# Optimization experiments

Measured on AMD Instinct MI355X. Metric: run time of the kernel, lower is better.

## Reference

```python
import jax, jax.numpy as jnp
import numpy as np

N_NODES = 100000
N_EDGES = 1600000
IN_C, HID_C, OUT_C = 128, 128, 40


def setup_inputs() -> dict:
    key = jax.random.key(0)
    ks = jax.random.split(key, 10)
    def lin(k, fin, fout):
        return jax.random.normal(k, (fin, fout), jnp.float32) / np.sqrt(fin).astype(np.float32)
    return {
        "x": jax.random.normal(ks[0], (N_NODES, IN_C), jnp.float32),
        "edge_index": jax.random.randint(ks[1], (2, N_EDGES), 0, N_NODES, jnp.int64),
        "W1a": lin(ks[2], IN_C, HID_C), "b1a": jnp.zeros((HID_C,), jnp.float32),
        "W1b": lin(ks[3], HID_C, HID_C), "b1b": jnp.zeros((HID_C,), jnp.float32),
        "W2a": lin(ks[4], HID_C, HID_C), "b2a": jnp.zeros((HID_C,), jnp.float32),
        "W2b": lin(ks[5], HID_C, OUT_C), "b2b": jnp.zeros((OUT_C,), jnp.float32),
    }


def gin_conv(x, edge_index, Wa, ba, Wb, bb):
    # GINConv with eps=0: h_i = MLP(x_i + sum_{j in N(i)} x_j)
    src, dst = edge_index[0], edge_index[1]
    agg = jax.ops.segment_sum(x[src], dst, num_segments=N_NODES)  # [N, C]
    h = x + agg
    h = jnp.maximum(h @ Wa + ba, 0.0)  # Linear + ReLU
    return h @ Wb + bb                 # Linear


def reference(x, edge_index, W1a, b1a, W1b, b1b, W2a, b2a, W2b, b2b):
    h = gin_conv(x, edge_index, W1a, b1a, W1b, b1b)
    h = jnp.maximum(h, 0.0)
    # dropout(p=0.5) treated as identity (eval mode / deterministic reference)
    h = gin_conv(h, edge_index, W2a, b2a, W2b, b2b)
    return jax.nn.log_softmax(h, axis=1)
```

## Files before the change

### kernel.cpp

```cpp
#include <hip/hip_runtime.h>

#define N_NODES 100000
#define N_EDGES 1600000
#define CH 128
#define OUTC 40
#define CAP 64
#define NBKT 98
#define BKT_CAP 18432
#define P1_EDGES 4096
#define ROW4 16
#define QROW2 16
#define QSCALE (6.5f / 127.0f)
#define QINV   (127.0f / 6.5f)
#define ZROW N_NODES

typedef __attribute__((ext_vector_type(8))) short bf16x8s;
typedef __attribute__((ext_vector_type(4))) float f32x4;

__device__ __forceinline__ unsigned short f2b_rne(float f) {
    union { float f; unsigned int u; } c; c.f = f;
    unsigned int r = (c.u + 0x7FFF + ((c.u >> 16) & 1)) >> 16;
    return (unsigned short)r;
}
__device__ __forceinline__ float b2f(unsigned short b) {
    union { float f; unsigned int u; } c; c.u = ((unsigned int)b) << 16;
    return c.f;
}
__device__ __forceinline__ int q8(float f) {
    return __float2int_rn(fminf(fmaxf(f * QINV, -127.f), 127.f));
}

__global__ __launch_bounds__(256) void conv_f32_bf16_i8(const float4* __restrict__ in,
                                                        ushort4* __restrict__ outb,
                                                        uint2* __restrict__ outq, int n8) {
    int i = blockIdx.x * 256 + threadIdx.x;
    if (i >= n8) return;
    float4 a = in[i * 2], b = in[i * 2 + 1];
    ushort4 o0, o1;
    o0.x = f2b_rne(a.x); o0.y = f2b_rne(a.y); o0.z = f2b_rne(a.z); o0.w = f2b_rne(a.w);
    o1.x = f2b_rne(b.x); o1.y = f2b_rne(b.y); o1.z = f2b_rne(b.z); o1.w = f2b_rne(b.w);
    outb[i * 2] = o0; outb[i * 2 + 1] = o1;
    uint2 q;
    q.x = (unsigned)((q8(a.x) + 128) & 0xFF) | (((unsigned)((q8(a.y) + 128) & 0xFF)) << 8) |
          (((unsigned)((q8(a.z) + 128) & 0xFF)) << 16) | (((unsigned)((q8(a.w) + 128) & 0xFF)) << 24);
    q.y = (unsigned)((q8(b.x) + 128) & 0xFF) | (((unsigned)((q8(b.y) + 128) & 0xFF)) << 8) |
          (((unsigned)((q8(b.z) + 128) & 0xFF)) << 16) | (((unsigned)((q8(b.w) + 128) & 0xFF)) << 24);
    outq[i] = q;
}

__global__ __launch_bounds__(256) void setup_misc(int* __restrict__ gcursor,
                                                  unsigned int* __restrict__ xq,
                                                  unsigned int* __restrict__ h1q) {
    int t = threadIdx.x;
    if (t < NBKT) gcursor[t] = 0;
    if (t >= 128 && t < 160) {
        int i = t - 128;
        xq[(size_t)ZROW * 32 + i] = 0x80808080u;
        h1q[(size_t)ZROW * 32 + i] = 0x80808080u;
    }
}

__global__ __launch_bounds__(256) void bin_edges(const int* __restrict__ esrc,
                                                 const int* __restrict__ edst,
                                                 int* __restrict__ gcursor,
                                                 unsigned int* __restrict__ bins) {
    __shared__ uint2 stage[P1_EDGES];
    __shared__ int lcnt[NBKT];
    __shared__ int lofs[NBKT];
    __shared__ int lpos[NBKT];
    __shared__ int gbase[NBKT];
    const int tid = threadIdx.x;
    const int e0 = blockIdx.x * P1_EDGES;

    for (int i = tid; i < NBKT; i += 256) lcnt[i] = 0;
    __syncthreads();

    int s[16], d[16];
#pragma unroll
    for (int i = 0; i < 16; ++i) {
        int e = e0 + i * 256 + tid;
        if (e < N_EDGES) { s[i] = esrc[e]; d[i] = edst[e]; }
        else d[i] = -1;
    }
#pragma unroll
    for (int i = 0; i < 16; ++i)
        if (d[i] >= 0) atomicAdd(&lcnt[d[i] >> 10], 1);
    __syncthreads();

    if (tid < NBKT) lofs[tid] = lcnt[tid];
    __syncthreads();
    for (int dd = 1; dd < NBKT; dd <<= 1) {
        int v = 0;
        if (tid < NBKT && tid >= dd) v = lofs[tid - dd];
        __syncthreads();
        if (tid < NBKT) lofs[tid] += v;
        __syncthreads();
    }
    if (tid < NBKT) {
        lpos[tid] = lofs[tid] - lcnt[tid];
        gbase[tid] = atomicAdd(&gcursor[tid], lcnt[tid]);
    }
    __syncthreads();

#pragma unroll
    for (int i = 0; i < 16; ++i) {
        if (d[i] >= 0) {
            int b = d[i] >> 10;
            int slot = atomicAdd(&lpos[b], 1);
            stage[slot] = make_uint2((unsigned)s[i], (unsigned)d[i]);
        }
    }
    __syncthreads();

    int total = lofs[NBKT - 1];
    for (int r = tid; r < total; r += 256) {
        uint2 rec = stage[r];
        int b = (int)(rec.y >> 10);
        int excl = lofs[b] - lcnt[b];
        int pos = gbase[b] + (r - excl);
        unsigned p = ((rec.y & 1023u) << 17) | rec.x;
        if (pos < BKT_CAP) bins[(size_t)b * BKT_CAP + pos] = p;
    }
}

__global__ __launch_bounds__(256) void build_from_bins(const unsigned int* __restrict__ bins,
                                                       const int* __restrict__ gcursor,
                                                       int* __restrict__ adj,
                                                       int* __restrict__ cnt) {
    __shared__ int lc[1024];
    const int b = blockIdx.x;
    const int tid = threadIdx.x;
    const int base = b << 10;
    for (int i = tid; i < 1024; i += 256) lc[i] = 0;
    __syncthreads();
    int n = gcursor[b]; if (n > BKT_CAP) n = BKT_CAP;
    const unsigned int* myb = bins + (size_t)b * BKT_CAP;
    for (int i = tid; i < n; i += 256) {
        unsigned p = myb[i];
        int local = (int)(p >> 17);
        int src = (int)(p & 0x1FFFFu);
        int slot = atomicAdd(&lc[local], 1);
        if (slot < CAP) adj[((base + local) << 6) + slot] = src;
    }
    __syncthreads();
    for (int i = tid; i < 1024; i += 256) {
        int node = base + i;
        if (node < N_NODES) {
            int dg = lc[i];
            cnt[node] = dg;
            int s0 = dg > CAP ? CAP : dg;
            int nr = (s0 + 15) & ~15;
            for (int s = s0; s < nr; ++s)
                adj[(node << 6) + s] = ZROW;
        }
    }
}

__global__ __launch_bounds__(256) void pack_w3(const float* __restrict__ W0,
                                               const float* __restrict__ W1,
                                               const float* __restrict__ W2,
                                               unsigned short* __restrict__ P0,
                                               unsigned short* __restrict__ P1,
                                               unsigned short* __restrict__ P2) {
    int t = blockIdx.x * 256 + threadIdx.x;
    if (t >= 3 * 2048) return;
    int which = t >> 11;
    int rem = t & 2047;
    int lane = rem & 63;
    int ks = (rem >> 6) & 3;
    int nt = rem >> 8;
    const float* W = which == 0 ? W0 : (which == 1 ? W1 : W2);
    unsigned short* P = which == 0 ? P0 : (which == 1 ? P1 : P2);
    int n = nt * 16 + (lane & 15);
    int kbase = ks * 32 + (lane >> 4) * 8;
    unsigned short* dst = P + ((nt * 4 + ks) * 64 + lane) * 8;
#pragma unroll
    for (int j = 0; j < 8; ++j)
        dst[j] = f2b_rne(W[(kbase + j) * CH + n]);
}

__global__ __launch_bounds__(256) void pack_wout(const float* __restrict__ W,
                                                 unsigned short* __restrict__ P) {
    int t = blockIdx.x * 256 + threadIdx.x;
    if (t >= 768) return;
    int nt = t >> 8, rem = t & 255;
    int ks = rem >> 6, lane = rem & 63;
    int n = nt * 16 + (lane & 15);
    int kbase = ks * 32 + (lane >> 4) * 8;
    unsigned short* dst = P + ((nt * 4 + ks) * 64 + lane) * 8;
#pragma unroll
    for (int j = 0; j < 8; ++j)
        dst[j] = (n < OUTC) ? f2b_rne(W[(kbase + j) * OUTC + n]) : (unsigned short)0;
}

template <bool FIXED>
__device__ __forceinline__ void gather_u8_body(const unsigned int* __restrict__ xq,
                                               const unsigned short* __restrict__ xb,
                                               const int* __restrict__ adj,
                                               const int* __restrict__ cnt,
                                               const unsigned int* __restrict__ hmax,
                                               unsigned short* __restrict__ agg) {
    int node = blockIdx.x * 4 + (threadIdx.x >> 6);
    int lane = threadIdx.x & 63;
    if (node >= N_NODES) return;
    int grp = lane >> 4, l16 = lane & 15;
    const uint2* q2 = reinterpret_cast<const uint2*>(xq);
    const uint4* f4 = reinterpret_cast<const uint4*>(xb);

    int deg = cnt[node];
    if (deg > CAP) deg = CAP;
    int nr = (deg + 15) & ~15;
    int nb = (lane < nr) ? adj[(node << 6) + lane] : 0;
    uint4 sv = f4[node * ROW4 + l16];

    float dq;
    if (FIXED) dq = QSCALE;
    else {
        union { unsigned u; float f; } c; c.u = hmax[0];
        dq = c.f * (1.0f / 127.0f);
    }

    unsigned a0 = 0, a1 = 0, a2 = 0, a3 = 0;

    for (int j = 0; j < nr; j += 16) {
        int j0 = j + grp;
        int s0 = __shfl(nb, j0, 64);
        int s1 = __shfl(nb, j0 + 4, 64);
        int s2 = __shfl(nb, j0 + 8, 64);
        int s3 = __shfl(nb, j0 + 12, 64);
        uint2 v0 = q2[s0 * QROW2 + l16];
        uint2 v1 = q2[s1 * QROW2 + l16];
        uint2 v2 = q2[s2 * QROW2 + l16];
        uint2 v3 = q2[s3 * QROW2 + l16];
        a0 += __builtin_amdgcn_perm(v0.x, v0.x, 0x0C020C00u);
        a1 += __builtin_amdgcn_perm(v0.x, v0.x, 0x0C030C01u);
        a2 += __builtin_amdgcn_perm(v0.y, v0.y, 0x0C020C00u);
        a3 += __builtin_amdgcn_perm(v0.y, v0.y, 0x0C030C01u);
        a0 += __builtin_amdgcn_perm(v1.x, v1.x, 0x0C020C00u);
        a1 += __builtin_amdgcn_perm(v1.x, v1.x, 0x0C030C01u);
        a2 += __builtin_amdgcn_perm(v1.y, v1.y, 0x0C020C00u);
        a3 += __builtin_amdgcn_perm(v1.y, v1.y, 0x0C030C01u);
        a0 += __builtin_amdgcn_perm(v2.x, v2.x, 0x0C020C00u);
        a1 += __builtin_amdgcn_perm(v2.x, v2.x, 0x0C030C01u);
        a2 += __builtin_amdgcn_perm(v2.y, v2.y, 0x0C020C00u);
        a3 += __builtin_amdgcn_perm(v2.y, v2.y, 0x0C030C01u);
        a0 += __builtin_amdgcn_perm(v3.x, v3.x, 0x0C020C00u);
        a1 += __builtin_amdgcn_perm(v3.x, v3.x, 0x0C030C01u);
        a2 += __builtin_amdgcn_perm(v3.y, v3.y, 0x0C020C00u);
        a3 += __builtin_amdgcn_perm(v3.y, v3.y, 0x0C030C01u);
    }
    a0 += (unsigned)__shfl_xor((int)a0, 16, 64); a0 += (unsigned)__shfl_xor((int)a0, 32, 64);
    a1 += (unsigned)__shfl_xor((int)a1, 16, 64); a1 += (unsigned)__shfl_xor((int)a1, 32, 64);
    a2 += (unsigned)__shfl_xor((int)a2, 16, 64); a2 += (unsigned)__shfl_xor((int)a2, 32, 64);
    a3 += (unsigned)__shfl_xor((int)a3, 16, 64); a3 += (unsigned)__shfl_xor((int)a3, 32, 64);

    if (grp == 0) {
        int bias = nr << 7;
        float q0 = (float)((int)(a0 & 0xFFFFu) - bias);
        float q1 = (float)((int)(a1 & 0xFFFFu) - bias);
        float q2c = (float)((int)(a0 >> 16) - bias);
        float q3 = (float)((int)(a1 >> 16) - bias);
        float q4 = (float)((int)(a2 & 0xFFFFu) - bias);
        float q5 = (float)((int)(a3 & 0xFFFFu) - bias);
        float q6 = (float)((int)(a2 >> 16) - bias);
        float q7 = (float)((int)(a3 >> 16) - bias);
        float r0 = b2f((unsigned short)(sv.x & 0xFFFF)) + dq * q0;
        float r1 = b2f((unsigned short)(sv.x >> 16)) + dq * q1;
        float r2 = b2f((unsigned short)(sv.y & 0xFFFF)) + dq * q2c;
        float r3 = b2f((unsigned short)(sv.y >> 16)) + dq * q3;
        float r4 = b2f((unsigned short)(sv.z & 0xFFFF)) + dq * q4;
        float r5 = b2f((unsigned short)(sv.z >> 16)) + dq * q5;
        float r6 = b2f((unsigned short)(sv.w & 0xFFFF)) + dq * q6;
        float r7 = b2f((unsigned short)(sv.w >> 16)) + dq * q7;
        uint4 o;
        o.x = (unsigned)f2b_rne(r0) | ((unsigned)f2b_rne(r1) << 16);
        o.y = (unsigned)f2b_rne(r2) | ((unsigned)f2b_rne(r3) << 16);
        o.z = (unsigned)f2b_rne(r4) | ((unsigned)f2b_rne(r5) << 16);
        o.w = (unsigned)f2b_rne(r6) | ((unsigned)f2b_rne(r7) << 16);
        reinterpret_cast<uint4*>(agg)[node * ROW4 + l16] = o;
    }
}

__global__ __launch_bounds__(256) void gather_agg_u8(const unsigned int* __restrict__ xq,
                                                     const unsigned short* __restrict__ xb,
                                                     const int* __restrict__ adj,
                                                     const int* __restrict__ cnt,
                                                     unsigned short* __restrict__ agg) {
    gather_u8_body<true>(xq, xb, adj, cnt, nullptr, agg);
}

__global__ __launch_bounds__(256) void gather_agg_u8_dyn(const unsigned int* __restrict__ xq,
                                                         const unsigned short* __restrict__ xb,
                                                         const int* __restrict__ adj,
                                                         const int* __restrict__ cnt,
                                                         const unsigned int* __restrict__ hmax,
                                                         unsigned short* __restrict__ agg) {
    gather_u8_body<false>(xq, xb, adj, cnt, hmax, agg);
}

__global__ __launch_bounds__(256) void reduce_max(const float* __restrict__ bmax, int n,
                                                  unsigned int* __restrict__ hmax) {
    float m = 0.f;
    for (int i = threadIdx.x; i < n; i += 256) m = fmaxf(m, bmax[i]);
#pragma unroll
    for (int off = 1; off < 64; off <<= 1) m = fmaxf(m, __shfl_xor(m, off, 64));
    __shared__ float wm[4];
    if ((threadIdx.x & 63) == 0) wm[threadIdx.x >> 6] = m;
    __syncthreads();
    if (threadIdx.x == 0)
        hmax[0] = __float_as_uint(fmaxf(fmaxf(wm[0], wm[1]), fmaxf(wm[2], wm[3])));
}

__global__ __launch_bounds__(256) void quant_h1(const uint4* __restrict__ h1,
                                                const unsigned int* __restrict__ hmax,
                                                uint2* __restrict__ outq, int n8) {
    int i = blockIdx.x * 256 + threadIdx.x;
    if (i >= n8) return;
    union { unsigned u; float f; } c; c.u = hmax[0];
    float inv = 127.0f / fmaxf(c.f, 1e-30f);
    uint4 v = h1[i];
    int q[8];
    q[0] = __float2int_rn(fminf(b2f((unsigned short)(v.x & 0xFFFF)) * inv, 127.f));
    q[1] = __float2int_rn(fminf(b2f((unsigned short)(v.x >> 16)) * inv, 127.f));
    q[2] = __float2int_rn(fminf(b2f((unsigned short)(v.y & 0xFFFF)) * inv, 127.f));
    q[3] = __float2int_rn(fminf(b2f((unsigned short)(v.y >> 16)) * inv, 127.f));
    q[4] = __float2int_rn(fminf(b2f((unsigned short)(v.z & 0xFFFF)) * inv, 127.f));
    q[5] = __float2int_rn(fminf(b2f((unsigned short)(v.z >> 16)) * inv, 127.f));
    q[6] = __float2int_rn(fminf(b2f((unsigned short)(v.w & 0xFFFF)) * inv, 127.f));
    q[7] = __float2int_rn(fminf(b2f((unsigned short)(v.w >> 16)) * inv, 127.f));
    uint2 o;
    o.x = (unsigned)((q[0] + 128) & 0xFF) | (((unsigned)((q[1] + 128) & 0xFF)) << 8) |
          (((unsigned)((q[2] + 128) & 0xFF)) << 16) | (((unsigned)((q[3] + 128) & 0xFF)) << 24);
    o.y = (unsigned)((q[4] + 128) & 0xFF) | (((unsigned)((q[5] + 128) & 0xFF)) << 8) |
          (((unsigned)((q[6] + 128) & 0xFF)) << 16) | (((unsigned)((q[7] + 128) & 0xFF)) << 24);
    outq[i] = o;
}

__global__ __launch_bounds__(256) void gin_mlp_fused(const unsigned short* __restrict__ A,
                                                     const unsigned short* __restrict__ Pa,
                                                     const float* __restrict__ ba,
                                                     const unsigned short* __restrict__ Pb2,
                                                     const float* __restrict__ bb,
                                                     unsigned short* __restrict__ Cout,
                                                     float* __restrict__ bmax,
                                                     int M) {
    __shared__ unsigned short As[64 * 136];
    __shared__ float sm_max[4];
    const int row0 = blockIdx.x * 64;
    const int tid = threadIdx.x;
    const int wave = tid >> 6;
    const int lane = tid & 63;
    const int quad = lane >> 4;
    const int l15 = lane & 15;
    const int nt0 = wave * 2;

    bf16x8s b1f[2][4];
#pragma unroll
    for (int c = 0; c < 2; ++c)
#pragma unroll
        for (int ks = 0; ks < 4; ++ks)
            b1f[c][ks] = *reinterpret_cast<const bf16x8s*>(
                Pa + (((nt0 + c) * 4 + ks) * 64 + lane) * 8);

    {
        int r = tid & 63, seg = tid >> 6;
        int row = row0 + r;
        uint4 z = make_uint4(0, 0, 0, 0);
        const uint4* src = reinterpret_cast<const uint4*>(A + (long long)row * CH + seg * 32);
        uint4* dst = reinterpret_cast<uint4*>(&As[r * 136 + seg * 32]);
#pragma unroll
        for (int i = 0; i < 4; ++i)
            dst[i] = (row < M) ? src[i] : z;
    }
    __syncthreads();

    f32x4 acc[2][4];
#pragma unroll
    for (int c = 0; c < 2; ++c)
#pragma unroll
        for (int t = 0; t < 4; ++t) acc[c][t] = (f32x4){0.f, 0.f, 0.f, 0.f};
#pragma unroll
    for (int t = 0; t < 4; ++t)
#pragma unroll
        for (int ks = 0; ks < 4; ++ks) {
            bf16x8s af = *reinterpret_cast<const bf16x8s*>(
                &As[(t * 16 + l15) * 136 + ks * 32 + quad * 8]);
            acc[0][t] = __builtin_amdgcn_mfma_f32_16x16x32_bf16(af, b1f[0][ks], acc[0][t], 0, 0, 0);
            acc[1][t] = __builtin_amdgcn_mfma_f32_16x16x32_bf16(af, b1f[1][ks], acc[1][t], 0, 0, 0);
        }

    bf16x8s b2f_[2][4];
#pragma unroll
    for (int c = 0; c < 2; ++c)
#pragma unroll
        for (int ks = 0; ks < 4; ++ks)
            b2f_[c][ks] = *reinterpret_cast<const bf16x8s*>(
                Pb2 + (((nt0 + c) * 4 + ks) * 64 + lane) * 8);

    __syncthreads();
#pragma unroll
    for (int c = 0; c < 2; ++c) {
        int col = (nt0 + c) * 16 + l15;
        float bv = ba[col];
#pragma unroll
        for (int t = 0; t < 4; ++t)
#pragma unroll
            for (int r = 0; r < 4; ++r) {
                int rl = t * 16 + quad * 4 + r;
                As[rl * 136 + col] = f2b_rne(fmaxf(acc[c][t][r] + bv, 0.f));
            }
    }
    __syncthreads();

    f32x4 a2[2][4];
#pragma unroll
    for (int c = 0; c < 2; ++c)
#pragma unroll
        for (int t = 0; t < 4; ++t) a2[c][t] = (f32x4){0.f, 0.f, 0.f, 0.f};
#pragma unroll
    for (int t = 0; t < 4; ++t)
#pragma unroll
        for (int ks = 0; ks < 4; ++ks) {
            bf16x8s af = *reinterpret_cast<const bf16x8s*>(
                &As[(t * 16 + l15) * 136 + ks * 32 + quad * 8]);
            a2[0][t] = __builtin_amdgcn_mfma_f32_16x16x32_bf16(af, b2f_[0][ks], a2[0][t], 0, 0, 0);
            a2[1][t] = __builtin_amdgcn_mfma_f32_16x16x32_bf16(af, b2f_[1][ks], a2[1][t], 0, 0, 0);
        }
    __syncthreads();

    float wmax = 0.f;
#pragma unroll
    for (int c = 0; c < 2; ++c) {
        int col = (nt0 + c) * 16 + l15;
        float bv = bb[col];
#pragma unroll
        for (int t = 0; t < 4; ++t)
#pragma unroll
            for (int r = 0; r < 4; ++r) {
                int rl = t * 16 + quad * 4 + r;
                float v = fmaxf(a2[c][t][r] + bv, 0.f);
                if (row0 + rl < M) wmax = fmaxf(wmax, v);
                As[rl * 136 + col] = f2b_rne(v);
            }
    }
#pragma unroll
    for (int off = 1; off < 64; off <<= 1) wmax = fmaxf(wmax, __shfl_xor(wmax, off, 64));
    if (lane == 0) sm_max[wave] = wmax;
    __syncthreads();

    {
        int r = tid >> 2;
        int q = tid & 3;
        int row = row0 + r;
        if (row < M) {
            uint4* dst = reinterpret_cast<uint4*>(Cout + (long long)row * CH + q * 32);
            const unsigned short* sp = &As[r * 136 + q * 32];
#pragma unroll
            for (int i = 0; i < 4; ++i)
                dst[i] = *reinterpret_cast<const uint4*>(sp + i * 8);
        }
        if (tid == 0)
            bmax[blockIdx.x] = fmaxf(fmaxf(sm_max[0], sm_max[1]),
                                     fmaxf(sm_max[2], sm_max[3]));
    }
}

__global__ __launch_bounds__(256) void gin_out_fused(const unsigned short* __restrict__ A,
                                                     const unsigned short* __restrict__ Pa,
                                                     const float* __restrict__ ba,
                                                     const unsigned short* __restrict__ Pb,
                                                     const float* __restrict__ bias,
                                                     float* __restrict__ out, int M) {
    __shared__ unsigned short As[64 * 136];
    const int row0 = blockIdx.x * 64;
    const int tid = threadIdx.x;
    const int wave = tid >> 6;
    const int lane = tid & 63;
    const int quad = lane >> 4;
    const int l15 = lane & 15;
    const int nt0 = wave * 2;

    bf16x8s b1f[2][4];
#pragma unroll
    for (int c = 0; c < 2; ++c)
#pragma unroll
        for (int ks = 0; ks < 4; ++ks)
            b1f[c][ks] = *reinterpret_cast<const bf16x8s*>(
                Pa + (((nt0 + c) * 4 + ks) * 64 + lane) * 8);

    {
        int r = tid & 63, seg = tid >> 6;
        int row = row0 + r;
        uint4 z = make_uint4(0, 0, 0, 0);
        const uint4* src = reinterpret_cast<const uint4*>(A + (long long)row * CH + seg * 32);
        uint4* dst = reinterpret_cast<uint4*>(&As[r * 136 + seg * 32]);
#pragma unroll
        for (int i = 0; i < 4; ++i)
            dst[i] = (row < M) ? src[i] : z;
    }
    __syncthreads();

    f32x4 acc[2][4];
#pragma unroll
    for (int c = 0; c < 2; ++c)
#pragma unroll
        for (int t = 0; t < 4; ++t) acc[c][t] = (f32x4){0.f, 0.f, 0.f, 0.f};
#pragma unroll
    for (int t = 0; t < 4; ++t)
#pragma unroll
        for (int ks = 0; ks < 4; ++ks) {
            bf16x8s af = *reinterpret_cast<const bf16x8s*>(
                &As[(t * 16 + l15) * 136 + ks * 32 + quad * 8]);
            acc[0][t] = __builtin_amdgcn_mfma_f32_16x16x32_bf16(af, b1f[0][ks], acc[0][t], 0, 0, 0);
            acc[1][t] = __builtin_amdgcn_mfma_f32_16x16x32_bf16(af, b1f[1][ks], acc[1][t], 0, 0, 0);
        }

    bf16x8s bof[3][4];
#pragma unroll
    for (int nt = 0; nt < 3; ++nt)
#pragma unroll
        for (int ks = 0; ks < 4; ++ks)
            bof[nt][ks] = *reinterpret_cast<const bf16x8s*>(
                Pb + ((nt * 4 + ks) * 64 + lane) * 8);

    __syncthreads();
#pragma unroll
    for (int c = 0; c < 2; ++c) {
        int col = (nt0 + c) * 16 + l15;
        float bv = ba[col];
#pragma unroll
        for (int t = 0; t < 4; ++t)
#pragma unroll
            for (int r = 0; r < 4; ++r) {
                int rl = t * 16 + quad * 4 + r;
                As[rl * 136 + col] = f2b_rne(fmaxf(acc[c][t][r] + bv, 0.f));
            }
    }
    __syncthreads();

    f32x4 oacc[3];
#pragma unroll
    for (int nt = 0; nt < 3; ++nt) oacc[nt] = (f32x4){0.f, 0.f, 0.f, 0.f};
#pragma unroll
    for (int ks = 0; ks < 4; ++ks) {
        bf16x8s af = *reinterpret_cast<const bf16x8s*>(
            &As[(wave * 16 + l15) * 136 + ks * 32 + quad * 8]);
#pragma unroll
        for (int nt = 0; nt < 3; ++nt)
            oacc[nt] = __builtin_amdgcn_mfma_f32_16x16x32_bf16(af, bof[nt][ks], oacc[nt], 0, 0, 0);
    }

    const float b0v = bias[l15];
    const float b1v = bias[16 + l15];
    const float b2v = (l15 < 8) ? bias[32 + l15] : 0.f;
#pragma unroll
    for (int r = 0; r < 4; ++r) {
        int row = row0 + wave * 16 + quad * 4 + r;
        float v0 = oacc[0][r] + b0v;
        float v1 = oacc[1][r] + b1v;
        float v2 = (l15 < 8) ? (oacc[2][r] + b2v) : -1e30f;
        float m = fmaxf(fmaxf(v0, v1), v2);
#pragma unroll
        for (int off = 1; off < 16; off <<= 1) m = fmaxf(m, __shfl_xor(m, off, 64));
        float s = __expf(v0 - m) + __expf(v1 - m) + ((l15 < 8) ? __expf(v2 - m) : 0.f);
#pragma unroll
        for (int off = 1; off < 16; off <<= 1) s += __shfl_xor(s, off, 64);
        float lg = m + __logf(s);
        if (row < M) {
            float* orow = out + (long long)row * OUTC;
            orow[l15] = v0 - lg;
            orow[16 + l15] = v1 - lg;
            if (l15 < 8) orow[32 + l15] = v2 - lg;
        }
    }
}

extern "C" void kernel_launch(void* const* d_in, const int* in_sizes, int n_in,
                              void* d_out, int out_size, void* d_ws, size_t ws_size,
                              hipStream_t stream) {
    const float* x   = (const float*)d_in[0];
    const int* eidx  = (const int*)d_in[1];
    const int* esrc  = eidx;
    const int* edst  = eidx + N_EDGES;
    const float* W1a = (const float*)d_in[2];
    const float* b1a = (const float*)d_in[3];
    const float* W1b = (const float*)d_in[4];
    const float* b1b = (const float*)d_in[5];
    const float* W2a = (const float*)d_in[6];
    const float* b2a = (const float*)d_in[7];
    const float* W2b = (const float*)d_in[8];
    const float* b2b = (const float*)d_in[9];
    float* out = (float*)d_out;

    const size_t fe = (size_t)N_NODES * CH;
    const size_t qrow_pad = 32;
    unsigned short* xb  = (unsigned short*)d_ws;
    unsigned short* b0  = xb + fe;
    unsigned short* b1  = b0 + fe;
    unsigned int* xq    = (unsigned int*)(b1 + fe);
    unsigned int* h1q   = xq + fe / 4 + qrow_pad;
    int* adj     = (int*)(h1q + fe / 4 + qrow_pad);
    int* cnt     = adj + (size_t)N_NODES * CAP;
    int* gcursor = cnt + N_NODES;
    unsigned int* hmax = (unsigned int*)(gcursor + NBKT);
    float* bmax = (float*)(hmax + 2);
    unsigned int* bins = (unsigned int*)(bmax + 1568);
    unsigned short* P1 = (unsigned short*)(bins + (size_t)NBKT * BKT_CAP);
    unsigned short* P2 = P1 + 16384;
    unsigned short* P3 = P2 + 16384;
    unsigned short* Pb = P3 + 16384;

    const int conv_grid  = (int)((fe / 8 + 255) / 256);
    const int bin_grid   = (N_EDGES + P1_EDGES - 1) / P1_EDGES;
    const int gath_grid  = (N_NODES + 3) / 4;
    const int gemm_grid  = (N_NODES + 63) / 64;
    const int q8_grid    = (int)((fe / 8 + 255) / 256);

    conv_f32_bf16_i8<<<conv_grid, 256, 0, stream>>>((const float4*)x, (ushort4*)xb,
                                                    (uint2*)xq, (int)(fe / 8));
    setup_misc<<<1, 256, 0, stream>>>(gcursor, xq, h1q);
    bin_edges<<<bin_grid, 256, 0, stream>>>(esrc, edst, gcursor, bins);
    build_from_bins<<<NBKT, 256, 0, stream>>>(bins, gcursor, adj, cnt);
    pack_w3<<<24, 256, 0, stream>>>(W1a, W1b, W2a, P1, P2, P3);
    pack_wout<<<3, 256, 0, stream>>>(W2b, Pb);

    gather_agg_u8<<<gath_grid, 256, 0, stream>>>(xq, xb, adj, cnt, b0);
    gin_mlp_fused<<<gemm_grid, 256, 0, stream>>>(b0, P1, b1a, P2, b1b, b1, bmax, N_NODES);

    reduce_max<<<1, 256, 0, stream>>>(bmax, gemm_grid, hmax);
    quant_h1<<<q8_grid, 256, 0, stream>>>((const uint4*)b1, hmax, (uint2*)h1q, (int)(fe / 8));
    gather_agg_u8_dyn<<<gath_grid, 256, 0, stream>>>(h1q, b1, adj, cnt, hmax, b0);
    gin_out_fused<<<gemm_grid, 256, 0, stream>>>(b0, P3, b2a, Pb, b2b, out, N_NODES);
}
```

Measured before the change: 299.9 us.

## Merge small setup kernels and gather two nodes per wave

Folds the setup_misc zeroing into block 0 of the conversion kernel. Merges the two weight-packing kernels into one and folds the global max reduction into every quant_h1 block, which removes three launches. build_from_bins now runs 1024 threads per bucket and no longer writes ZROW padding, because the gather masks lanes at or beyond the degree to ZROW itself. The gather processes two nodes per wave to raise memory-level parallelism. The cost is that each quant_h1 block re-reads all block maxima, and the pair loop runs to the larger of the two degrees.

```diff
diff --git a/kernel.cpp b/kernel.cpp
--- a/kernel.cpp
+++ b/kernel.cpp
@@ -32,7 +32,19 @@
 
 __global__ __launch_bounds__(256) void conv_f32_bf16_i8(const float4* __restrict__ in,
                                                         ushort4* __restrict__ outb,
-                                                        uint2* __restrict__ outq, int n8) {
+                                                        uint2* __restrict__ outq, int n8,
+                                                        int* __restrict__ gcursor,
+                                                        unsigned int* __restrict__ xqd,
+                                                        unsigned int* __restrict__ h1qd) {
+    if (blockIdx.x == 0) {
+        int t = threadIdx.x;
+        if (t < NBKT) gcursor[t] = 0;
+        if (t >= 128 && t < 160) {
+            int i = t - 128;
+            xqd[(size_t)ZROW * 32 + i] = 0x80808080u;
+            h1qd[(size_t)ZROW * 32 + i] = 0x80808080u;
+        }
+    }
     int i = blockIdx.x * 256 + threadIdx.x;
     if (i >= n8) return;
     float4 a = in[i * 2], b = in[i * 2 + 1];
@@ -48,18 +60,6 @@
     outq[i] = q;
 }
 
-__global__ __launch_bounds__(256) void setup_misc(int* __restrict__ gcursor,
-                                                  unsigned int* __restrict__ xq,
-                                                  unsigned int* __restrict__ h1q) {
-    int t = threadIdx.x;
-    if (t < NBKT) gcursor[t] = 0;
-    if (t >= 128 && t < 160) {
-        int i = t - 128;
-        xq[(size_t)ZROW * 32 + i] = 0x80808080u;
-        h1q[(size_t)ZROW * 32 + i] = 0x80808080u;
-    }
-}
-
 __global__ __launch_bounds__(256) void bin_edges(const int* __restrict__ esrc,
                                                  const int* __restrict__ edst,
                                                  int* __restrict__ gcursor,
@@ -123,19 +123,19 @@
     }
 }
 
-__global__ __launch_bounds__(256) void build_from_bins(const unsigned int* __restrict__ bins,
-                                                       const int* __restrict__ gcursor,
-                                                       int* __restrict__ adj,
-                                                       int* __restrict__ cnt) {
+__global__ __launch_bounds__(1024) void build_from_bins(const unsigned int* __restrict__ bins,
+                                                        const int* __restrict__ gcursor,
+                                                        int* __restrict__ adj,
+                                                        int* __restrict__ cnt) {
     __shared__ int lc[1024];
     const int b = blockIdx.x;
     const int tid = threadIdx.x;
     const int base = b << 10;
-    for (int i = tid; i < 1024; i += 256) lc[i] = 0;
+    lc[tid] = 0;
     __syncthreads();
     int n = gcursor[b]; if (n > BKT_CAP) n = BKT_CAP;
     const unsigned int* myb = bins + (size_t)b * BKT_CAP;
-    for (int i = tid; i < n; i += 256) {
+    for (int i = tid; i < n; i += 1024) {
         unsigned p = myb[i];
         int local = (int)(p >> 17);
         int src = (int)(p & 0x1FFFFu);
@@ -143,54 +143,72 @@
         if (slot < CAP) adj[((base + local) << 6) + slot] = src;
     }
     __syncthreads();
-    for (int i = tid; i < 1024; i += 256) {
-        int node = base + i;
-        if (node < N_NODES) {
-            int dg = lc[i];
-            cnt[node] = dg;
-            int s0 = dg > CAP ? CAP : dg;
-            int nr = (s0 + 15) & ~15;
-            for (int s = s0; s < nr; ++s)
-                adj[(node << 6) + s] = ZROW;
-        }
-    }
-}
-
-__global__ __launch_bounds__(256) void pack_w3(const float* __restrict__ W0,
-                                               const float* __restrict__ W1,
-                                               const float* __restrict__ W2,
-                                               unsigned short* __restrict__ P0,
-                                               unsigned short* __restrict__ P1,
-                                               unsigned short* __restrict__ P2) {
+    {
+        int node = base + tid;
+        if (node < N_NODES) cnt[node] = lc[tid];
+    }
+}
+
+__global__ __launch_bounds__(256) void pack_weights(const float* __restrict__ W0,
+                                                    const float* __restrict__ W1,
+                                                    const float* __restrict__ W2,
+                                                    const float* __restrict__ Wo,
+                                                    unsigned short* __restrict__ P0,
+                                                    unsigned short* __restrict__ P1,
+                                                    unsigned short* __restrict__ P2,
+                                                    unsigned short* __restrict__ Po) {
     int t = blockIdx.x * 256 + threadIdx.x;
-    if (t >= 3 * 2048) return;
-    int which = t >> 11;
-    int rem = t & 2047;
-    int lane = rem & 63;
-    int ks = (rem >> 6) & 3;
-    int nt = rem >> 8;
-    const float* W = which == 0 ? W0 : (which == 1 ? W1 : W2);
-    unsigned short* P = which == 0 ? P0 : (which == 1 ? P1 : P2);
-    int n = nt * 16 + (lane & 15);
-    int kbase = ks * 32 + (lane >> 4) * 8;
-    unsigned short* dst = P + ((nt * 4 + ks) * 64 + lane) * 8;
-#pragma unroll
-    for (int j = 0; j < 8; ++j)
-        dst[j] = f2b_rne(W[(kbase + j) * CH + n]);
-}
-
-__global__ __launch_bounds__(256) void pack_wout(const float* __restrict__ W,
-                                                 unsigned short* __restrict__ P) {
-    int t = blockIdx.x * 256 + threadIdx.x;
-    if (t >= 768) return;
-    int nt = t >> 8, rem = t & 255;
-    int ks = rem >> 6, lane = rem & 63;
-    int n = nt * 16 + (lane & 15);
-    int kbase = ks * 32 + (lane >> 4) * 8;
-    unsigned short* dst = P + ((nt * 4 + ks) * 64 + lane) * 8;
-#pragma unroll
-    for (int j = 0; j < 8; ++j)
-        dst[j] = (n < OUTC) ? f2b_rne(W[(kbase + j) * OUTC + n]) : (unsigned short)0;
+    if (t < 3 * 2048) {
+        int which = t >> 11;
+        int rem = t & 2047;
+        int lane = rem & 63;
+        int ks = (rem >> 6) & 3;
+        int nt = rem >> 8;
+        const float* W = which == 0 ? W0 : (which == 1 ? W1 : W2);
+        unsigned short* P = which == 0 ? P0 : (which == 1 ? P1 : P2);
+        int n = nt * 16 + (lane & 15);
+        int kbase = ks * 32 + (lane >> 4) * 8;
+        unsigned short* dst = P + ((nt * 4 + ks) * 64 + lane) * 8;
+#pragma unroll
+        for (int j = 0; j < 8; ++j)
+            dst[j] = f2b_rne(W[(kbase + j) * CH + n]);
+    } else if (t < 3 * 2048 + 768) {
+        int u = t - 3 * 2048;
+        int nt = u >> 8, rem = u & 255;
+        int ks = rem >> 6, lane = rem & 63;
+        int n = nt * 16 + (lane & 15);
+        int kbase = ks * 32 + (lane >> 4) * 8;
+        unsigned short* dst = Po + ((nt * 4 + ks) * 64 + lane) * 8;
+#pragma unroll
+        for (int j = 0; j < 8; ++j)
+            dst[j] = (n < OUTC) ? f2b_rne(Wo[(kbase + j) * OUTC + n]) : (unsigned short)0;
+    }
+}
+
+__device__ __forceinline__ void gather_epi(unsigned a0, unsigned a1, unsigned a2, unsigned a3,
+                                           uint4 sv, int bias, float dq, uint4* __restrict__ dst) {
+    float q0 = (float)((int)(a0 & 0xFFFFu) - bias);
+    float q1 = (float)((int)(a1 & 0xFFFFu) - bias);
+    float q2 = (float)((int)(a0 >> 16) - bias);
+    float q3 = (float)((int)(a1 >> 16) - bias);
+    float q4 = (float)((int)(a2 & 0xFFFFu) - bias);
+    float q5 = (float)((int)(a3 & 0xFFFFu) - bias);
+    float q6 = (float)((int)(a2 >> 16) - bias);
+    float q7 = (float)((int)(a3 >> 16) - bias);
+    float r0 = b2f((unsigned short)(sv.x & 0xFFFF)) + dq * q0;
+    float r1 = b2f((unsigned short)(sv.x >> 16)) + dq * q1;
+    float r2 = b2f((unsigned short)(sv.y & 0xFFFF)) + dq * q2;
+    float r3 = b2f((unsigned short)(sv.y >> 16)) + dq * q3;
+    float r4 = b2f((unsigned short)(sv.z & 0xFFFF)) + dq * q4;
+    float r5 = b2f((unsigned short)(sv.z >> 16)) + dq * q5;
+    float r6 = b2f((unsigned short)(sv.w & 0xFFFF)) + dq * q6;
+    float r7 = b2f((unsigned short)(sv.w >> 16)) + dq * q7;
+    uint4 o;
+    o.x = (unsigned)f2b_rne(r0) | ((unsigned)f2b_rne(r1) << 16);
+    o.y = (unsigned)f2b_rne(r2) | ((unsigned)f2b_rne(r3) << 16);
+    o.z = (unsigned)f2b_rne(r4) | ((unsigned)f2b_rne(r5) << 16);
+    o.w = (unsigned)f2b_rne(r6) | ((unsigned)f2b_rne(r7) << 16);
+    *dst = o;
 }
 
 template <bool FIXED>
@@ -200,18 +218,24 @@
                                                const int* __restrict__ cnt,
                                                const unsigned int* __restrict__ hmax,
                                                unsigned short* __restrict__ agg) {
-    int node = blockIdx.x * 4 + (threadIdx.x >> 6);
-    int lane = threadIdx.x & 63;
-    if (node >= N_NODES) return;
-    int grp = lane >> 4, l16 = lane & 15;
+    const int wave = threadIdx.x >> 6;
+    const int lane = threadIdx.x & 63;
+    const int node0 = blockIdx.x * 8 + wave * 2;
+    if (node0 >= N_NODES) return;
+    const int grp = lane >> 4, l16 = lane & 15;
     const uint2* q2 = reinterpret_cast<const uint2*>(xq);
     const uint4* f4 = reinterpret_cast<const uint4*>(xb);
 
-    int deg = cnt[node];
-    if (deg > CAP) deg = CAP;
-    int nr = (deg + 15) & ~15;
-    int nb = (lane < nr) ? adj[(node << 6) + lane] : 0;
-    uint4 sv = f4[node * ROW4 + l16];
+    int2 dgp = *reinterpret_cast<const int2*>(cnt + node0);
+    int deg0 = dgp.x > CAP ? CAP : dgp.x;
+    int deg1 = dgp.y > CAP ? CAP : dgp.y;
+    int nr0 = (deg0 + 15) & ~15;
+    int nr1 = (deg1 + 15) & ~15;
+    int nrm = nr0 > nr1 ? nr0 : nr1;
+    int nb0 = (lane < deg0) ? adj[(node0 << 6) + lane] : ZROW;
+    int nb1 = (lane < deg1) ? adj[(node0 << 6) + 64 + lane] : ZROW;
+    uint4 sv0 = f4[node0 * ROW4 + l16];
+    uint4 sv1 = f4[node0 * ROW4 + ROW4 + l16];
 
     float dq;
     if (FIXED) dq = QSCALE;
@@ -220,64 +244,74 @@
         dq = c.f * (1.0f / 127.0f);
     }
 
-    unsigned a0 = 0, a1 = 0, a2 = 0, a3 = 0;
-
-    for (int j = 0; j < nr; j += 16) {
+    unsigned a00 = 0, a01 = 0, a02 = 0, a03 = 0;
+    unsigned a10 = 0, a11 = 0, a12 = 0, a13 = 0;
+
+    for (int j = 0; j < nrm; j += 16) {
         int j0 = j + grp;
-        int s0 = __shfl(nb, j0, 64);
-        int s1 = __shfl(nb, j0 + 4, 64);
-        int s2 = __shfl(nb, j0 + 8, 64);
-        int s3 = __shfl(nb, j0 + 12, 64);
-        uint2 v0 = q2[s0 * QROW2 + l16];
-        uint2 v1 = q2[s1 * QROW2 + l16];
-        uint2 v2 = q2[s2 * QROW2 + l16];
-        uint2 v3 = q2[s3 * QROW2 + l16];
-        a0 += __builtin_amdgcn_perm(v0.x, v0.x, 0x0C020C00u);
-        a1 += __builtin_amdgcn_perm(v0.x, v0.x, 0x0C030C01u);
-        a2 += __builtin_amdgcn_perm(v0.y, v0.y, 0x0C020C00u);
-        a3 += __builtin_amdgcn_perm(v0.y, v0.y, 0x0C030C01u);
-        a0 += __builtin_amdgcn_perm(v1.x, v1.x, 0x0C020C00u);
-        a1 += __builtin_amdgcn_perm(v1.x, v1.x, 0x0C030C01u);
-        a2 += __builtin_amdgcn_perm(v1.y, v1.y, 0x0C020C00u);
-        a3 += __builtin_amdgcn_perm(v1.y, v1.y, 0x0C030C01u);
-        a0 += __builtin_amdgcn_perm(v2.x, v2.x, 0x0C020C00u);
-        a1 += __builtin_amdgcn_perm(v2.x, v2.x, 0x0C030C01u);
-        a2 += __builtin_amdgcn_perm(v2.y, v2.y, 0x0C020C00u);
-        a3 += __builtin_amdgcn_perm(v2.y, v2.y, 0x0C030C01u);
-        a0 += __builtin_amdgcn_perm(v3.x, v3.x, 0x0C020C00u);
-        a1 += __builtin_amdgcn_perm(v3.x, v3.x, 0x0C030C01u);
-        a2 += __builtin_amdgcn_perm(v3.y, v3.y, 0x0C020C00u);
-        a3 += __builtin_amdgcn_perm(v3.y, v3.y, 0x0C030C01u);
-    }
-    a0 += (unsigned)__shfl_xor((int)a0, 16, 64); a0 += (unsigned)__shfl_xor((int)a0, 32, 64);
-    a1 += (unsigned)__shfl_xor((int)a1, 16, 64); a1 += (unsigned)__shfl_xor((int)a1, 32, 64);
-    a2 += (unsigned)__shfl_xor((int)a2, 16, 64); a2 += (unsigned)__shfl_xor((int)a2, 32, 64);
-    a3 += (unsigned)__shfl_xor((int)a3, 16, 64); a3 += (unsigned)__shfl_xor((int)a3, 32, 64);
+        int s00 = __shfl(nb0, j0, 64);
+        int s01 = __shfl(nb0, j0 + 4, 64);
+        int s02 = __shfl(nb0, j0 + 8, 64);
+        int s03 = __shfl(nb0, j0 + 12, 64);
+        int s10 = __shfl(nb1, j0, 64);
+        int s11 = __shfl(nb1, j0 + 4, 64);
+        int s12 = __shfl(nb1, j0 + 8, 64);
+        int s13 = __shfl(nb1, j0 + 12, 64);
+        uint2 v00 = q2[s00 * QROW2 + l16];
+        uint2 v01 = q2[s01 * QROW2 + l16];
+        uint2 v02 = q2[s02 * QROW2 + l16];
+        uint2 v03 = q2[s03 * QROW2 + l16];
+        uint2 v10 = q2[s10 * QROW2 + l16];
+        uint2 v11 = q2[s11 * QROW2 + l16];
+        uint2 v12 = q2[s12 * QROW2 + l16];
+        uint2 v13 = q2[s13 * QROW2 + l16];
+        a00 += __builtin_amdgcn_perm(v00.x, v00.x, 0x0C020C00u);
+        a01 += __builtin_amdgcn_perm(v00.x, v00.x, 0x0C030C01u);
+        a02 += __builtin_amdgcn_perm(v00.y, v00.y, 0x0C020C00u);
+        a03 += __builtin_amdgcn_perm(v00.y, v00.y, 0x0C030C01u);
+        a00 += __builtin_amdgcn_perm(v01.x, v01.x, 0x0C020C00u);
+        a01 += __builtin_amdgcn_perm(v01.x, v01.x, 0x0C030C01u);
+        a02 += __builtin_amdgcn_perm(v01.y, v01.y, 0x0C020C00u);
+        a03 += __builtin_amdgcn_perm(v01.y, v01.y, 0x0C030C01u);
+        a00 += __builtin_amdgcn_perm(v02.x, v02.x, 0x0C020C00u);
+        a01 += __builtin_amdgcn_perm(v02.x, v02.x, 0x0C030C01u);
+        a02 += __builtin_amdgcn_perm(v02.y, v02.y, 0x0C020C00u);
+        a03 += __builtin_amdgcn_perm(v02.y, v02.y, 0x0C030C01u);
+        a00 += __builtin_amdgcn_perm(v03.x, v03.x, 0x0C020C00u);
+        a01 += __builtin_amdgcn_perm(v03.x, v03.x, 0x0C030C01u);
+        a02 += __builtin_amdgcn_perm(v03.y, v03.y, 0x0C020C00u);
+        a03 += __builtin_amdgcn_perm(v03.y, v03.y, 0x0C030C01u);
+        a10 += __builtin_amdgcn_perm(v10.x, v10.x, 0x0C020C00u);
+        a11 += __builtin_amdgcn_perm(v10.x, v10.x, 0x0C030C01u);
+        a12 += __builtin_amdgcn_perm(v10.y, v10.y, 0x0C020C00u);
+        a13 += __builtin_amdgcn_perm(v10.y, v10.y, 0x0C030C01u);
+        a10 += __builtin_amdgcn_perm(v11.x, v11.x, 0x0C020C00u);
+        a11 += __builtin_amdgcn_perm(v11.x, v11.x, 0x0C030C01u);
+        a12 += __builtin_amdgcn_perm(v11.y, v11.y, 0x0C020C00u);
+        a13 += __builtin_amdgcn_perm(v11.y, v11.y, 0x0C030C01u);
+        a10 += __builtin_amdgcn_perm(v12.x, v12.x, 0x0C020C00u);
+        a11 += __builtin_amdgcn_perm(v12.x, v12.x, 0x0C030C01u);
+        a12 += __builtin_amdgcn_perm(v12.y, v12.y, 0x0C020C00u);
+        a13 += __builtin_amdgcn_perm(v12.y, v12.y, 0x0C030C01u);
+        a10 += __builtin_amdgcn_perm(v13.x, v13.x, 0x0C020C00u);
+        a11 += __builtin_amdgcn_perm(v13.x, v13.x, 0x0C030C01u);
+        a12 += __builtin_amdgcn_perm(v13.y, v13.y, 0x0C020C00u);
+        a13 += __builtin_amdgcn_perm(v13.y, v13.y, 0x0C030C01u);
+    }
+    a00 += (unsigned)__shfl_xor((int)a00, 16, 64); a00 += (unsigned)__shfl_xor((int)a00, 32, 64);
+    a01 += (unsigned)__shfl_xor((int)a01, 16, 64); a01 += (unsigned)__shfl_xor((int)a01, 32, 64);
+    a02 += (unsigned)__shfl_xor((int)a02, 16, 64); a02 += (unsigned)__shfl_xor((int)a02, 32, 64);
+    a03 += (unsigned)__shfl_xor((int)a03, 16, 64); a03 += (unsigned)__shfl_xor((int)a03, 32, 64);
+    a10 += (unsigned)__shfl_xor((int)a10, 16, 64); a10 += (unsigned)__shfl_xor((int)a10, 32, 64);
+    a11 += (unsigned)__shfl_xor((int)a11, 16, 64); a11 += (unsigned)__shfl_xor((int)a11, 32, 64);
+    a12 += (unsigned)__shfl_xor((int)a12, 16, 64); a12 += (unsigned)__shfl_xor((int)a12, 32, 64);
+    a13 += (unsigned)__shfl_xor((int)a13, 16, 64); a13 += (unsigned)__shfl_xor((int)a13, 32, 64);
 
     if (grp == 0) {
-        int bias = nr << 7;
-        float q0 = (float)((int)(a0 & 0xFFFFu) - bias);
-        float q1 = (float)((int)(a1 & 0xFFFFu) - bias);
-        float q2c = (float)((int)(a0 >> 16) - bias);
-        float q3 = (float)((int)(a1 >> 16) - bias);
-        float q4 = (float)((int)(a2 & 0xFFFFu) - bias);
-        float q5 = (float)((int)(a3 & 0xFFFFu) - bias);
-        float q6 = (float)((int)(a2 >> 16) - bias);
-        float q7 = (float)((int)(a3 >> 16) - bias);
-        float r0 = b2f((unsigned short)(sv.x & 0xFFFF)) + dq * q0;
-        float r1 = b2f((unsigned short)(sv.x >> 16)) + dq * q1;
-        float r2 = b2f((unsigned short)(sv.y & 0xFFFF)) + dq * q2c;
-        float r3 = b2f((unsigned short)(sv.y >> 16)) + dq * q3;
-        float r4 = b2f((unsigned short)(sv.z & 0xFFFF)) + dq * q4;
-        float r5 = b2f((unsigned short)(sv.z >> 16)) + dq * q5;
-        float r6 = b2f((unsigned short)(sv.w & 0xFFFF)) + dq * q6;
-        float r7 = b2f((unsigned short)(sv.w >> 16)) + dq * q7;
-        uint4 o;
-        o.x = (unsigned)f2b_rne(r0) | ((unsigned)f2b_rne(r1) << 16);
-        o.y = (unsigned)f2b_rne(r2) | ((unsigned)f2b_rne(r3) << 16);
-        o.z = (unsigned)f2b_rne(r4) | ((unsigned)f2b_rne(r5) << 16);
-        o.w = (unsigned)f2b_rne(r6) | ((unsigned)f2b_rne(r7) << 16);
-        reinterpret_cast<uint4*>(agg)[node * ROW4 + l16] = o;
+        int bias = nrm << 7;
+        uint4* dst = reinterpret_cast<uint4*>(agg);
+        gather_epi(a00, a01, a02, a03, sv0, bias, dq, dst + node0 * ROW4 + l16);
+        gather_epi(a10, a11, a12, a13, sv1, bias, dq, dst + node0 * ROW4 + ROW4 + l16);
     }
 }
 
@@ -298,26 +332,22 @@
     gather_u8_body<false>(xq, xb, adj, cnt, hmax, agg);
 }
 
-__global__ __launch_bounds__(256) void reduce_max(const float* __restrict__ bmax, int n,
-                                                  unsigned int* __restrict__ hmax) {
+__global__ __launch_bounds__(256) void quant_h1(const uint4* __restrict__ h1,
+                                                const float* __restrict__ bmax, int nbm,
+                                                unsigned int* __restrict__ hmax,
+                                                uint2* __restrict__ outq, int n8) {
+    __shared__ float wm[4];
     float m = 0.f;
-    for (int i = threadIdx.x; i < n; i += 256) m = fmaxf(m, bmax[i]);
+    for (int i = threadIdx.x; i < nbm; i += 256) m = fmaxf(m, bmax[i]);
 #pragma unroll
     for (int off = 1; off < 64; off <<= 1) m = fmaxf(m, __shfl_xor(m, off, 64));
-    __shared__ float wm[4];
     if ((threadIdx.x & 63) == 0) wm[threadIdx.x >> 6] = m;
     __syncthreads();
-    if (threadIdx.x == 0)
-        hmax[0] = __float_as_uint(fmaxf(fmaxf(wm[0], wm[1]), fmaxf(wm[2], wm[3])));
-}
-
-__global__ __launch_bounds__(256) void quant_h1(const uint4* __restrict__ h1,
-                                                const unsigned int* __restrict__ hmax,
-                                                uint2* __restrict__ outq, int n8) {
+    float hm = fmaxf(fmaxf(wm[0], wm[1]), fmaxf(wm[2], wm[3]));
+    if (blockIdx.x == 0 && threadIdx.x == 0) hmax[0] = __float_as_uint(hm);
     int i = blockIdx.x * 256 + threadIdx.x;
     if (i >= n8) return;
-    union { unsigned u; float f; } c; c.u = hmax[0];
-    float inv = 127.0f / fmaxf(c.f, 1e-30f);
+    float inv = 127.0f / fmaxf(hm, 1e-30f);
     uint4 v = h1[i];
     int q[8];
     q[0] = __float2int_rn(fminf(b2f((unsigned short)(v.x & 0xFFFF)) * inv, 127.f));
@@ -612,23 +642,22 @@
 
     const int conv_grid  = (int)((fe / 8 + 255) / 256);
     const int bin_grid   = (N_EDGES + P1_EDGES - 1) / P1_EDGES;
-    const int gath_grid  = (N_NODES + 3) / 4;
+    const int gath_grid  = (N_NODES + 7) / 8;
     const int gemm_grid  = (N_NODES + 63) / 64;
     const int q8_grid    = (int)((fe / 8 + 255) / 256);
 
     conv_f32_bf16_i8<<<conv_grid, 256, 0, stream>>>((const float4*)x, (ushort4*)xb,
-                                                    (uint2*)xq, (int)(fe / 8));
-    setup_misc<<<1, 256, 0, stream>>>(gcursor, xq, h1q);
+                                                    (uint2*)xq, (int)(fe / 8),
+                                                    gcursor, xq, h1q);
     bin_edges<<<bin_grid, 256, 0, stream>>>(esrc, edst, gcursor, bins);
-    build_from_bins<<<NBKT, 256, 0, stream>>>(bins, gcursor, adj, cnt);
-    pack_w3<<<24, 256, 0, stream>>>(W1a, W1b, W2a, P1, P2, P3);
-    pack_wout<<<3, 256, 0, stream>>>(W2b, Pb);
+    build_from_bins<<<NBKT, 1024, 0, stream>>>(bins, gcursor, adj, cnt);
+    pack_weights<<<27, 256, 0, stream>>>(W1a, W1b, W2a, W2b, P1, P2, P3, Pb);
 
     gather_agg_u8<<<gath_grid, 256, 0, stream>>>(xq, xb, adj, cnt, b0);
     gin_mlp_fused<<<gemm_grid, 256, 0, stream>>>(b0, P1, b1a, P2, b1b, b1, bmax, N_NODES);
 
-    reduce_max<<<1, 256, 0, stream>>>(bmax, gemm_grid, hmax);
-    quant_h1<<<q8_grid, 256, 0, stream>>>((const uint4*)b1, hmax, (uint2*)h1q, (int)(fe / 8));
+    quant_h1<<<q8_grid, 256, 0, stream>>>((const uint4*)b1, bmax, gemm_grid, hmax,
+                                          (uint2*)h1q, (int)(fe / 8));
     gather_agg_u8_dyn<<<gath_grid, 256, 0, stream>>>(h1q, b1, adj, cnt, hmax, b0);
     gin_out_fused<<<gemm_grid, 256, 0, stream>>>(b0, P3, b2a, Pb, b2b, out, N_NODES);
 }
```

Result: faster. 275.9 us (-8.0%).
